# Kernel optimization log

Hardware: AMD Instinct MI355X
Metric: run time of the kernel (lower is better)

## Reference

```python
import jax, jax.numpy as jnp
import numpy as np

T, B, IN, H = 512, 64, 256, 1024
LN_EPS = 1e-5


def _uniform(key, shape, fan_in):
    bound = 1.0 / np.sqrt(fan_in)
    return jax.random.uniform(key, shape, jnp.float32, -bound, bound)


def setup_inputs() -> dict:
    key = jax.random.key(0)
    ks = jax.random.split(key, 8)
    return {
        "x": jax.random.normal(ks[0], (T, B, IN), jnp.float32),
        "Wproj": _uniform(ks[1], (IN, H), IN),          # input_projection (no bias)
        "Wx0": _uniform(ks[2], (IN, 4 * H), IN),        # layer-0 input weights
        "Wh0": _uniform(ks[3], (H, 4 * H), H),          # layer-0 hidden weights
        "b0": _uniform(ks[4], (4 * H,), H),             # combined input+hidden bias
        "Wx1": _uniform(ks[5], (H, 4 * H), H),
        "Wh1": _uniform(ks[6], (H, 4 * H), H),
        "b1": _uniform(ks[7], (4 * H,), H),
        # per-layer LayerNorm params: [num_layers=2, H]
        "lnc_g": jnp.ones((2, H), jnp.float32), "lnc_b": jnp.zeros((2, H), jnp.float32),
        "lnh_g": jnp.ones((2, H), jnp.float32), "lnh_b": jnp.zeros((2, H), jnp.float32),
        "lno_g": jnp.ones((2, H), jnp.float32), "lno_b": jnp.zeros((2, H), jnp.float32),
    }


def _ln(v, g, b):
    m = jnp.mean(v, axis=-1, keepdims=True)
    var = jnp.mean((v - m) ** 2, axis=-1, keepdims=True)
    return (v - m) * jax.lax.rsqrt(var + LN_EPS) * g + b


def reference(x, Wproj, Wx0, Wh0, b0, Wx1, Wh1, b1,
              lnc_g, lnc_b, lnh_g, lnh_b, lno_g, lno_b):
    def cell(inp, h, c, Wx, Wh, bias, l):
        gates = inp @ Wx + h @ Wh + bias            # [B, 4H]
        i, f, g, o = jnp.split(gates, 4, axis=-1)
        c = jax.nn.sigmoid(f) * c + jnp.exp(i) * jnp.tanh(g)  # exponential input gate
        c = _ln(c, lnc_g[l], lnc_b[l])
        h = jax.nn.sigmoid(o) * jnp.tanh(c)
        h = _ln(h, lnh_g[l], lnh_b[l])
        return h, c

    def step(carry, xt):
        h0, c0, h1, c1 = carry
        # layer 0: cell -> residual (projected input) -> outer LayerNorm
        h0, c0 = cell(xt, h0, c0, Wx0, Wh0, b0, 0)
        h0 = _ln(h0 + xt @ Wproj, lno_g[0], lno_b[0])
        # layer 1: cell -> identity residual -> outer LayerNorm
        h1, c1 = cell(h0, h1, c1, Wx1, Wh1, b1, 1)
        h1 = _ln(h1 + h0, lno_g[1], lno_b[1])
        return (h0, c0, h1, c1), h1

    z = jnp.zeros((x.shape[1], H), x.dtype)
    (h0, c0, h1, c1), output = jax.lax.scan(step, (z, z, z, z), x)
    h_final = jnp.stack([h0, h1])  # [num_layers, B, H]
    c_final = jnp.stack([c0, c1])
    return output, h_final, c_final
```

## Files before the change

kernel.cpp:

```cpp
#include <hip/hip_runtime.h>
#include <math.h>

#define TSTEPS 512
#define BSZ    64
#define INDIM  256
#define HDIM   1024
#define G4     4096
#define NX     5120
#define LN_EPS 1e-5f

#define NBLK   256
#define NTHR   1024
#define CHUNK  8
#define CROWS  (CHUNK * BSZ)
#define NCHUNK (TSTEPS / CHUNK)
#define HRING  16
#define HSLOT  65536

#define LDS_LDK    2054
#define LDS_LO_OFF (16 * LDS_LDK)
#define LDS_W_BYTES (2 * 16 * LDS_LDK * 2)
#define LDS_STG_OFF LDS_W_BYTES
#define LDS_RED_OFF (LDS_W_BYTES + 4096)
#define LDS_GST_OFF (LDS_RED_OFF + 256)
#define LDS_BYTES   (LDS_GST_OFF + 16384)

typedef short          s8v __attribute__((ext_vector_type(8)));
typedef float          f4v __attribute__((ext_vector_type(4)));
typedef unsigned short u16;

#define MFMA __builtin_amdgcn_mfma_f32_16x16x32_bf16

__device__ __forceinline__ u16 f2bf(float f) {
    unsigned u = __float_as_uint(f);
    u += 0x7FFFu + ((u >> 16) & 1u);
    return (u16)(u >> 16);
}
__device__ __forceinline__ float bf2f(u16 h) {
    return __uint_as_float(((unsigned)h) << 16);
}
__device__ __forceinline__ float sigm(float x) { return 1.f / (1.f + expf(-x)); }

__device__ __forceinline__ float aldf(const float* p) {
    unsigned v = __hip_atomic_load((unsigned*)p, __ATOMIC_RELAXED,
                                   __HIP_MEMORY_SCOPE_AGENT);
    return __uint_as_float(v);
}
__device__ __forceinline__ void ast16B(u16* p, s8v v) {
    asm volatile("global_store_dwordx4 %0, %1, off sc1"
                 :: "v"(p), "v"(v) : "memory");
}
__device__ __forceinline__ void ast16Bf(float* p, f4v v) {
    asm volatile("global_store_dwordx4 %0, %1, off sc1"
                 :: "v"(p), "v"(v) : "memory");
}

__device__ __forceinline__ void store_c_16B(float* stgw, int lane, f4v acc,
                                            float* dst, int ld)
{
    const int row = lane & 15, kg = lane >> 4;
#pragma unroll
    for (int r = 0; r < 4; ++r)
        stgw[(kg * 4 + r) * 16 + row] = acc[r];
    f4v v = *(f4v*)(stgw + lane * 4);
    ast16Bf(dst + (lane >> 2) * ld + (lane & 3) * 4, v);
}

#define GSTRIDE 512
__device__ __forceinline__ void grid_barrier(int* bar, int nbar, bool fence)
{
    asm volatile("s_waitcnt vmcnt(0)" ::: "memory");
    __syncthreads();
    if (threadIdx.x == 0) {
        const int g = blockIdx.x & 15;
        int* gctr = bar + g * GSTRIDE;
        int* ggo  = gctr + 32;
        int* root = bar + 16 * GSTRIDE;
        int v = __hip_atomic_fetch_add(gctr, 1, __ATOMIC_RELAXED,
                                       __HIP_MEMORY_SCOPE_AGENT);
        if (v == nbar * 16 - 1) {
            int rv = __hip_atomic_fetch_add(root, 1, __ATOMIC_RELAXED,
                                            __HIP_MEMORY_SCOPE_AGENT);
            if (rv == nbar * 16 - 1) {
#pragma unroll
                for (int g2 = 0; g2 < 16; ++g2)
                    __hip_atomic_store(bar + g2 * GSTRIDE + 32, nbar,
                                       __ATOMIC_RELAXED, __HIP_MEMORY_SCOPE_AGENT);
            }
        }
        while (__hip_atomic_load(ggo, __ATOMIC_RELAXED,
                                 __HIP_MEMORY_SCOPE_AGENT) < nbar) {}
        if (fence)
            __builtin_amdgcn_fence(__ATOMIC_ACQUIRE, "agent");
        asm volatile("" ::: "memory");
    }
    __syncthreads();
}

__device__ __forceinline__ void taskA(int g, int lane, float* stgw,
    const u16* __restrict__ h0hi_s, const u16* __restrict__ h0lo_s,
    const u16* __restrict__ Whthi, const u16* __restrict__ Whtlo,
    float* __restrict__ parts0)
{
    const int ks = g & 1, tile = g >> 1;
    const int rt = tile & 3, ct = tile >> 2;
    const int row = lane & 15, kg = lane >> 4;
    const int m = rt * 16 + row;
    const u16* wh = Whthi + (size_t)(ct * 16 + row) * HDIM + ks * 512 + kg * 8;
    const u16* wl = Whtlo + (size_t)(ct * 16 + row) * HDIM + ks * 512 + kg * 8;
    const u16* ah = h0hi_s + (size_t)m * HDIM + ks * 512 + kg * 8;
    const u16* al = h0lo_s + (size_t)m * HDIM + ks * 512 + kg * 8;
    f4v acc = {0.f, 0.f, 0.f, 0.f};
    s8v Ah = *(const s8v*)(ah);
    s8v Al = *(const s8v*)(al);
    s8v Bh = *(const s8v*)(wh);
    s8v Bl = *(const s8v*)(wl);
#pragma unroll
    for (int i = 0; i < 16; ++i) {
        s8v nAh, nAl, nBh, nBl;
        if (i + 1 < 16) {
            const int kn = (i + 1) * 32;
            nAh = *(const s8v*)(ah + kn);
            nAl = *(const s8v*)(al + kn);
            nBh = *(const s8v*)(wh + kn);
            nBl = *(const s8v*)(wl + kn);
        }
        acc = MFMA(Ah, Bh, acc, 0, 0, 0);
        acc = MFMA(Ah, Bl, acc, 0, 0, 0);
        acc = MFMA(Al, Bh, acc, 0, 0, 0);
        Ah = nAh; Al = nAl; Bh = nBh; Bl = nBl;
    }
    store_c_16B(stgw, lane, acc,
                parts0 + (size_t)ks * BSZ * G4 + (size_t)(rt * 16) * G4 + ct * 16,
                G4);
}

__device__ __forceinline__ void taskX(int task, int c, int lane, float* stgw,
    const u16* __restrict__ xhi, const u16* __restrict__ xlo,
    const u16* __restrict__ Wxthi, const u16* __restrict__ Wxtlo,
    float* __restrict__ xgbuf)
{
    const int mt = task & 31, ct = task >> 5;
    const int row = lane & 15, kg = lane >> 4;
    const int mr = mt * 16 + row;
    const u16* ah = xhi + ((size_t)c * CROWS + mr) * INDIM + kg * 8;
    const u16* al = xlo + ((size_t)c * CROWS + mr) * INDIM + kg * 8;
    const u16* wh = Wxthi + (size_t)(ct * 16 + row) * INDIM + kg * 8;
    const u16* wl = Wxtlo + (size_t)(ct * 16 + row) * INDIM + kg * 8;
    f4v acc = {0.f, 0.f, 0.f, 0.f};
    s8v Ah = *(const s8v*)(ah);
    s8v Al = *(const s8v*)(al);
    s8v Bh = *(const s8v*)(wh);
    s8v Bl = *(const s8v*)(wl);
#pragma unroll
    for (int i = 0; i < 8; ++i) {
        s8v nAh, nAl, nBh, nBl;
        if (i + 1 < 8) {
            const int kn = (i + 1) * 32;
            nAh = *(const s8v*)(ah + kn);
            nAl = *(const s8v*)(al + kn);
            nBh = *(const s8v*)(wh + kn);
            nBl = *(const s8v*)(wl + kn);
        }
        acc = MFMA(Ah, Bh, acc, 0, 0, 0);
        acc = MFMA(Ah, Bl, acc, 0, 0, 0);
        acc = MFMA(Al, Bh, acc, 0, 0, 0);
        Ah = nAh; Al = nAl; Bh = nBh; Bl = nBl;
    }
    store_c_16B(stgw, lane, acc,
                xgbuf + (size_t)(mt * 16) * NX + ct * 16, NX);
}

__device__ __forceinline__ void taskC(int blk, int wv, int lane, float* stgw,
    const u16* __restrict__ shW,
    const u16* __restrict__ h0hi_s, const u16* __restrict__ h0lo_s,
    const u16* __restrict__ h1hi_s, const u16* __restrict__ h1lo_s,
    float* __restrict__ parts1)
{
    const int rt = wv & 3, hs = wv >> 2;
    const int row = lane & 15, kg = lane >> 4;
    const int m = rt * 16 + row;
    const u16* ah0 = (hs ? h1hi_s : h0hi_s) + (size_t)m * HDIM + kg * 8;
    const u16* al0 = (hs ? h1lo_s : h0lo_s) + (size_t)m * HDIM + kg * 8;
    const u16* sh  = shW + row * LDS_LDK + hs * 1024 + kg * 8;
    const u16* sl  = shW + LDS_LO_OFF + row * LDS_LDK + hs * 1024 + kg * 8;
    f4v acc = {0.f, 0.f, 0.f, 0.f};
    s8v Ah = *(const s8v*)(ah0);
    s8v Al = *(const s8v*)(al0);
#pragma unroll
    for (int i = 0; i < 32; ++i) {
        s8v nAh, nAl;
        if (i + 1 < 32) {
            nAh = *(const s8v*)(ah0 + (i + 1) * 32);
            nAl = *(const s8v*)(al0 + (i + 1) * 32);
        }
        const int kloc = i * 32;
        s8v Bh = *(const s8v*)(sh + kloc);
        s8v Bl = *(const s8v*)(sl + kloc);
        acc = MFMA(Ah, Bh, acc, 0, 0, 0);
        acc = MFMA(Ah, Bl, acc, 0, 0, 0);
        acc = MFMA(Al, Bh, acc, 0, 0, 0);
        Ah = nAh; Al = nAl;
    }
    store_c_16B(stgw, lane, acc,
                parts1 + (size_t)hs * BSZ * G4 + (size_t)(rt * 16) * G4 + blk * 16,
                G4);
}

__device__ __forceinline__ float2 blk_sum2(float s, float q, float* red, int tid)
{
#pragma unroll
    for (int off = 32; off; off >>= 1) {
        s += __shfl_down(s, off);
        q += __shfl_down(q, off);
    }
    if ((tid & 63) == 0) { red[(tid >> 6) * 2] = s; red[(tid >> 6) * 2 + 1] = q; }
    __syncthreads();
    float ts = 0.f, tq = 0.f;
#pragma unroll
    for (int i = 0; i < 16; ++i) { ts += red[2 * i]; tq += red[2 * i + 1]; }
    __syncthreads();
    return make_float2(ts, tq);
}

__device__ __forceinline__ float lnorm(float v, float2 sq, float g, float b)
{
    float mean = sq.x * (1.f / 1024.f);
    float var  = sq.y * (1.f / 1024.f) - mean * mean;
    return (v - mean) * rsqrtf(var + LN_EPS) * g + b;
}

__device__ __forceinline__ void store_h_16B(u16* stg, int tid,
                                            u16 hi, u16 lo,
                                            u16* dhi, u16* dlo, int base)
{
    stg[tid] = hi;
    stg[1024 + tid] = lo;
    __syncthreads();
    if (tid < 256) {
        const u16* src = stg + (tid >> 7) * 1024 + (tid & 127) * 8;
        s8v v = *(const s8v*)src;
        u16* dst = ((tid >> 7) == 0 ? dhi : dlo) + base + (tid & 127) * 8;
        ast16B(dst, v);
    }
    __syncthreads();
}

__global__ __launch_bounds__(NTHR, 4) void persistent(
    const u16* __restrict__ xhi,  const u16* __restrict__ xlo,
    const u16* __restrict__ Whthi, const u16* __restrict__ Whtlo,
    const u16* __restrict__ Wxthi, const u16* __restrict__ Wxtlo,
    const u16* __restrict__ W1thi, const u16* __restrict__ W1tlo,
    const float* __restrict__ b0, const float* __restrict__ b1,
    const float* __restrict__ lncg, const float* __restrict__ lncb,
    const float* __restrict__ lnhg, const float* __restrict__ lnhb,
    const float* __restrict__ lnog, const float* __restrict__ lnob,
    float* __restrict__ xg,
    float* __restrict__ parts0,
    float* __restrict__ parts1,
    u16* __restrict__ h0hi, u16* __restrict__ h0lo,
    u16* __restrict__ h1hi, u16* __restrict__ h1lo,
    float* __restrict__ out, int* bar)
{
    extern __shared__ char smem[];
    u16*   shW   = (u16*)smem;
    u16*   stg   = (u16*)(smem + LDS_STG_OFF);
    float* red   = (float*)(smem + LDS_RED_OFF);
    float* stg_g = (float*)(smem + LDS_GST_OFF);

    const int blk  = blockIdx.x;
    const int tid  = threadIdx.x;
    const int wv   = tid >> 6;
    const int lane = tid & 63;
    float* stgw = stg_g + wv * 256;
    int nbar = 0;

    float c0reg = 0.f, h0reg = 0.f, c1reg = 0.f, h1reg = 0.f;

    {
        const size_t gcol = (size_t)(blk * 16 + wv) * 2048;
        for (int j = lane * 8; j < 2048; j += 512) {
            *(s8v*)(shW + wv * LDS_LDK + j)              = *(const s8v*)(W1thi + gcol + j);
            *(s8v*)(shW + LDS_LO_OFF + wv * LDS_LDK + j) = *(const s8v*)(W1tlo + gcol + j);
        }
    }
    grid_barrier(bar, ++nbar, false);

    {
        const int g = blk * 16 + wv;
        for (int task = g; task < 10240; task += 4096)
            taskX(task, 0, lane, stgw, xhi, xlo, Wxthi, Wxtlo, xg);
    }
    grid_barrier(bar, ++nbar, false);

    for (int t = 0; t < TSTEPS; ++t) {
        const int s0  = t & (HRING - 1);
        const int s0p = (t - 1) & (HRING - 1);
        const int s1p = (t - 1) & (HRING - 1);
        const bool fence = ((t & 7) == 7);

        if (blk < 64) {
            const int b = blk, n = tid;
            const float* XG = xg + (size_t)((t >> 3) & 1) * CROWS * NX
                                 + (size_t)((t & 7) * BSZ + b) * NX;
            const float* P0 = parts0 + (size_t)b * G4;
            const float* P1 = parts0 + (size_t)(BSZ + b) * G4;
            float gi = aldf(&XG[n])        + aldf(&P0[n])        + aldf(&P1[n])        + b0[n];
            float gf = aldf(&XG[1024 + n]) + aldf(&P0[1024 + n]) + aldf(&P1[1024 + n]) + b0[1024 + n];
            float gg = aldf(&XG[2048 + n]) + aldf(&P0[2048 + n]) + aldf(&P1[2048 + n]) + b0[2048 + n];
            float go = aldf(&XG[3072 + n]) + aldf(&P0[3072 + n]) + aldf(&P1[3072 + n]) + b0[3072 + n];
            float xp = aldf(&XG[4096 + n]);
            float cv = sigm(gf) * c0reg + expf(gi) * tanhf(gg);
            float2 r = blk_sum2(cv, cv * cv, red, tid);
            float cl = lnorm(cv, r, lncg[n], lncb[n]);
            c0reg = cl;
            float hv = sigm(go) * tanhf(cl);
            r = blk_sum2(hv, hv * hv, red, tid);
            float hl = lnorm(hv, r, lnhg[n], lnhb[n]) + xp;
            r = blk_sum2(hl, hl * hl, red, tid);
            float hn = lnorm(hl, r, lnog[n], lnob[n]);
            h0reg = hn;
            u16 hi = f2bf(hn);
            store_h_16B(stg, tid, hi, f2bf(hn - bf2f(hi)),
                        h0hi + (size_t)s0 * HSLOT, h0lo + (size_t)s0 * HSLOT,
                        b * HDIM);
        } else if (blk < 128) {
            if (t > 0) {
                const int b = blk - 64, n = tid;
                const float* P0 = parts1 + (size_t)b * G4;
                const float* P1 = parts1 + (size_t)(BSZ + b) * G4;
                float gi = aldf(&P0[n])        + aldf(&P1[n])        + b1[n];
                float gf = aldf(&P0[1024 + n]) + aldf(&P1[1024 + n]) + b1[1024 + n];
                float gg = aldf(&P0[2048 + n]) + aldf(&P1[2048 + n]) + b1[2048 + n];
                float go = aldf(&P0[3072 + n]) + aldf(&P1[3072 + n]) + b1[3072 + n];
                float cv = sigm(gf) * c1reg + expf(gi) * tanhf(gg);
                float2 r = blk_sum2(cv, cv * cv, red, tid);
                float cl = lnorm(cv, r, lncg[HDIM + n], lncb[HDIM + n]);
                c1reg = cl;
                float hv = sigm(go) * tanhf(cl);
                r = blk_sum2(hv, hv * hv, red, tid);
                float h0v = bf2f(h0hi[(size_t)s0p * HSLOT + b * HDIM + n])
                          + bf2f(h0lo[(size_t)s0p * HSLOT + b * HDIM + n]);
                float hl = lnorm(hv, r, lnhg[HDIM + n], lnhb[HDIM + n]) + h0v;
                r = blk_sum2(hl, hl * hl, red, tid);
                float hn = lnorm(hl, r, lnog[HDIM + n], lnob[HDIM + n]);
                h1reg = hn;
                u16 hi = f2bf(hn);
                out[(size_t)(t - 1) * BSZ * HDIM + b * HDIM + n] = hn;
                store_h_16B(stg, tid, hi, f2bf(hn - bf2f(hi)),
                            h1hi + (size_t)s1p * HSLOT, h1lo + (size_t)s1p * HSLOT,
                            b * HDIM);
            }
        } else {
            const int c = (t >> 3) + 1;
            if (c < NCHUNK) {
                float* xgbuf = xg + (size_t)(c & 1) * CROWS * NX;
                const int widx = (blk - 128) * 16 + wv;
                if (widx < 1280)
                    taskX((t & 7) * 1280 + widx, c, lane, stgw,
                          xhi, xlo, Wxthi, Wxtlo, xgbuf);
            }
        }
        grid_barrier(bar, ++nbar, false);

        if (wv < 8) {
            taskC(blk, wv, lane, stgw, shW,
                  h0hi + (size_t)s0 * HSLOT,  h0lo + (size_t)s0 * HSLOT,
                  h1hi + (size_t)s1p * HSLOT, h1lo + (size_t)s1p * HSLOT,
                  parts1);
        } else if (t + 1 < TSTEPS) {
            taskA(blk * 8 + (wv - 8), lane, stgw,
                  h0hi + (size_t)s0 * HSLOT, h0lo + (size_t)s0 * HSLOT,
                  Whthi, Whtlo, parts0);
        }
        grid_barrier(bar, ++nbar, fence);
    }

    if (blk >= 64 && blk < 128) {
        const int b = blk - 64, n = tid;
        const int tp = TSTEPS - 1;
        const int sp = tp & (HRING - 1);
        const float* P0 = parts1 + (size_t)b * G4;
        const float* P1 = parts1 + (size_t)(BSZ + b) * G4;
        float gi = aldf(&P0[n])        + aldf(&P1[n])        + b1[n];
        float gf = aldf(&P0[1024 + n]) + aldf(&P1[1024 + n]) + b1[1024 + n];
        float gg = aldf(&P0[2048 + n]) + aldf(&P1[2048 + n]) + b1[2048 + n];
        float go = aldf(&P0[3072 + n]) + aldf(&P1[3072 + n]) + b1[3072 + n];
        float cv = sigm(gf) * c1reg + expf(gi) * tanhf(gg);
        float2 r = blk_sum2(cv, cv * cv, red, tid);
        float cl = lnorm(cv, r, lncg[HDIM + n], lncb[HDIM + n]);
        c1reg = cl;
        float hv = sigm(go) * tanhf(cl);
        r = blk_sum2(hv, hv * hv, red, tid);
        float h0v = bf2f(h0hi[(size_t)sp * HSLOT + b * HDIM + n])
                  + bf2f(h0lo[(size_t)sp * HSLOT + b * HDIM + n]);
        float hl = lnorm(hv, r, lnhg[HDIM + n], lnhb[HDIM + n]) + h0v;
        r = blk_sum2(hl, hl * hl, red, tid);
        float hn = lnorm(hl, r, lnog[HDIM + n], lnob[HDIM + n]);
        h1reg = hn;
        out[(size_t)tp * BSZ * HDIM + b * HDIM + n] = hn;
    }

    {
        const size_t F = (size_t)TSTEPS * BSZ * HDIM;
        if (blk < 64) {
            out[F +          blk * HDIM + tid] = h0reg;
            out[F + 131072 + blk * HDIM + tid] = c0reg;
        } else if (blk < 128) {
            const int b = blk - 64;
            out[F +  65536 + b * HDIM + tid] = h1reg;
            out[F + 196608 + b * HDIM + tid] = c1reg;
        }
    }
}

__global__ __launch_bounds__(256) void transpose_split(
    const float* __restrict__ src, int N,
    u16* __restrict__ dsthi, u16* __restrict__ dstlo,
    int ldd, int noff, int koff)
{
    __shared__ float tile[32][33];
    const int n0 = blockIdx.x * 32, k0 = blockIdx.y * 32;
    const int tx = threadIdx.x & 31, ty = threadIdx.x >> 5;
#pragma unroll
    for (int i = 0; i < 4; ++i)
        tile[ty + i * 8][tx] = src[(size_t)(k0 + ty + i * 8) * N + n0 + tx];
    __syncthreads();
#pragma unroll
    for (int i = 0; i < 4; ++i) {
        float v = tile[tx][ty + i * 8];
        u16 hi = f2bf(v);
        u16 lo = f2bf(v - bf2f(hi));
        size_t idx = (size_t)(n0 + ty + i * 8 + noff) * ldd + k0 + koff + tx;
        dsthi[idx] = hi;
        dstlo[idx] = lo;
    }
}

__global__ void conv_split(const float* __restrict__ src,
                           u16* __restrict__ hi, u16* __restrict__ lo, int n4)
{
    int i = blockIdx.x * 256 + threadIdx.x;
    if (i < n4) {
        float4 v = ((const float4*)src)[i];
        ushort4 h, l;
        h.x = f2bf(v.x); l.x = f2bf(v.x - bf2f(h.x));
        h.y = f2bf(v.y); l.y = f2bf(v.y - bf2f(h.y));
        h.z = f2bf(v.z); l.z = f2bf(v.z - bf2f(h.z));
        h.w = f2bf(v.w); l.w = f2bf(v.w - bf2f(h.w));
        ((ushort4*)hi)[i] = h;
        ((ushort4*)lo)[i] = l;
    }
}

extern "C" void kernel_launch(void* const* d_in, const int* in_sizes, int n_in,
                              void* d_out, int out_size, void* d_ws, size_t ws_size,
                              hipStream_t stream)
{
    const float* x     = (const float*)d_in[0];
    const float* Wproj = (const float*)d_in[1];
    const float* Wx0   = (const float*)d_in[2];
    const float* Wh0   = (const float*)d_in[3];
    const float* b0    = (const float*)d_in[4];
    const float* Wx1   = (const float*)d_in[5];
    const float* Wh1   = (const float*)d_in[6];
    const float* b1    = (const float*)d_in[7];
    const float* lnc_g = (const float*)d_in[8];
    const float* lnc_b = (const float*)d_in[9];
    const float* lnh_g = (const float*)d_in[10];
    const float* lnh_b = (const float*)d_in[11];
    const float* lno_g = (const float*)d_in[12];
    const float* lno_b = (const float*)d_in[13];
    float* out = (float*)d_out;

    char* base = (char*)d_ws;
    size_t o = 0;
    u16* x_hi  = (u16*)(base + o); o += (size_t)TSTEPS * BSZ * INDIM * 2;
    u16* x_lo  = (u16*)(base + o); o += (size_t)TSTEPS * BSZ * INDIM * 2;
    u16* Whthi = (u16*)(base + o); o += (size_t)G4 * HDIM * 2;
    u16* Whtlo = (u16*)(base + o); o += (size_t)G4 * HDIM * 2;
    u16* Wxthi = (u16*)(base + o); o += (size_t)NX * INDIM * 2;
    u16* Wxtlo = (u16*)(base + o); o += (size_t)NX * INDIM * 2;
    u16* W1thi = (u16*)(base + o); o += (size_t)G4 * 2048 * 2;
    u16* W1tlo = (u16*)(base + o); o += (size_t)G4 * 2048 * 2;
    float* xg     = (float*)(base + o); o += (size_t)2 * CROWS * NX * 4;
    float* parts0 = (float*)(base + o); o += (size_t)2 * BSZ * G4 * 4;
    float* parts1 = (float*)(base + o); o += (size_t)2 * BSZ * G4 * 4;
    u16* h0hi = (u16*)(base + o); o += (size_t)HRING * HSLOT * 2;
    u16* h0lo = (u16*)(base + o); o += (size_t)HRING * HSLOT * 2;
    u16* h1hi = (u16*)(base + o); o += (size_t)HRING * HSLOT * 2;
    u16* h1lo = (u16*)(base + o); o += (size_t)HRING * HSLOT * 2;
    int* bar  = (int*)(base + o); o += 40960;
    if (ws_size < o) return;

    conv_split<<<dim3(8192), 256, 0, stream>>>(x, x_hi, x_lo, 2097152);
    transpose_split<<<dim3(128, 32), 256, 0, stream>>>(Wh0, G4, Whthi, Whtlo, HDIM, 0, 0);
    transpose_split<<<dim3(128, 8),  256, 0, stream>>>(Wx0,   G4,   Wxthi, Wxtlo, INDIM, 0,    0);
    transpose_split<<<dim3(32, 8),   256, 0, stream>>>(Wproj, HDIM, Wxthi, Wxtlo, INDIM, 4096, 0);
    transpose_split<<<dim3(128, 32), 256, 0, stream>>>(Wx1, G4, W1thi, W1tlo, 2048, 0, 0);
    transpose_split<<<dim3(128, 32), 256, 0, stream>>>(Wh1, G4, W1thi, W1tlo, 2048, 0, 1024);
    hipMemsetAsync(parts0, 0, (size_t)2 * BSZ * G4 * 4, stream);
    hipMemsetAsync(h0hi, 0, (size_t)4 * HRING * HSLOT * 2, stream);
    hipMemsetAsync(bar, 0, 40960, stream);

    persistent<<<dim3(NBLK), dim3(NTHR), LDS_BYTES, stream>>>(
        x_hi, x_lo, Whthi, Whtlo, Wxthi, Wxtlo, W1thi, W1tlo, b0, b1,
        lnc_g, lnc_b, lnh_g, lnh_b, lno_g, lno_b,
        xg, parts0, parts1,
        h0hi, h0lo, h1hi, h1lo, out, bar);
}
```

Measured before the change: 25.35 ms.

## Drop split-K partials and fold x-projection tasks into the MFMA phase

The recurrent matmuls for both layers now have each wave compute the full K dimension into a single partial buffer, instead of two split-K halves. The elementwise phase therefore loads one partial per gate rather than two. The x-gate precompute work moves from the blocks that were idle during elementwise (blocks 128+) onto waves 8-15 of every block in the matmul phase. This frees those waves' time and removes the extra partial reads. The cost is longer per-wave MFMA chains and less parallelism per tile. Memory fences now run every 16 steps instead of every 8, and the output write uses nontemporal stores.

```diff
diff --git a/kernel.cpp b/kernel.cpp
--- a/kernel.cpp
+++ b/kernel.cpp
@@ -97,28 +97,26 @@
     __syncthreads();
 }
 
-__device__ __forceinline__ void taskA(int g, int lane, float* stgw,
+__device__ __forceinline__ void taskA(int blk, int rt, int lane, float* stgw,
     const u16* __restrict__ h0hi_s, const u16* __restrict__ h0lo_s,
     const u16* __restrict__ Whthi, const u16* __restrict__ Whtlo,
     float* __restrict__ parts0)
 {
-    const int ks = g & 1, tile = g >> 1;
-    const int rt = tile & 3, ct = tile >> 2;
     const int row = lane & 15, kg = lane >> 4;
     const int m = rt * 16 + row;
-    const u16* wh = Whthi + (size_t)(ct * 16 + row) * HDIM + ks * 512 + kg * 8;
-    const u16* wl = Whtlo + (size_t)(ct * 16 + row) * HDIM + ks * 512 + kg * 8;
-    const u16* ah = h0hi_s + (size_t)m * HDIM + ks * 512 + kg * 8;
-    const u16* al = h0lo_s + (size_t)m * HDIM + ks * 512 + kg * 8;
+    const u16* wh = Whthi + (size_t)(blk * 16 + row) * HDIM + kg * 8;
+    const u16* wl = Whtlo + (size_t)(blk * 16 + row) * HDIM + kg * 8;
+    const u16* ah = h0hi_s + (size_t)m * HDIM + kg * 8;
+    const u16* al = h0lo_s + (size_t)m * HDIM + kg * 8;
     f4v acc = {0.f, 0.f, 0.f, 0.f};
     s8v Ah = *(const s8v*)(ah);
     s8v Al = *(const s8v*)(al);
     s8v Bh = *(const s8v*)(wh);
     s8v Bl = *(const s8v*)(wl);
 #pragma unroll
-    for (int i = 0; i < 16; ++i) {
+    for (int i = 0; i < 32; ++i) {
         s8v nAh, nAl, nBh, nBl;
-        if (i + 1 < 16) {
+        if (i + 1 < 32) {
             const int kn = (i + 1) * 32;
             nAh = *(const s8v*)(ah + kn);
             nAl = *(const s8v*)(al + kn);
@@ -131,8 +129,7 @@
         Ah = nAh; Al = nAl; Bh = nBh; Bl = nBl;
     }
     store_c_16B(stgw, lane, acc,
-                parts0 + (size_t)ks * BSZ * G4 + (size_t)(rt * 16) * G4 + ct * 16,
-                G4);
+                parts0 + (size_t)(rt * 16) * G4 + blk * 16, G4);
 }
 
 __device__ __forceinline__ void taskX(int task, int c, int lane, float* stgw,
@@ -171,40 +168,41 @@
                 xgbuf + (size_t)(mt * 16) * NX + ct * 16, NX);
 }
 
-__device__ __forceinline__ void taskC(int blk, int wv, int lane, float* stgw,
+__device__ __forceinline__ void taskC(int blk, int rt, int lane, float* stgw,
     const u16* __restrict__ shW,
     const u16* __restrict__ h0hi_s, const u16* __restrict__ h0lo_s,
     const u16* __restrict__ h1hi_s, const u16* __restrict__ h1lo_s,
     float* __restrict__ parts1)
 {
-    const int rt = wv & 3, hs = wv >> 2;
     const int row = lane & 15, kg = lane >> 4;
     const int m = rt * 16 + row;
-    const u16* ah0 = (hs ? h1hi_s : h0hi_s) + (size_t)m * HDIM + kg * 8;
-    const u16* al0 = (hs ? h1lo_s : h0lo_s) + (size_t)m * HDIM + kg * 8;
-    const u16* sh  = shW + row * LDS_LDK + hs * 1024 + kg * 8;
-    const u16* sl  = shW + LDS_LO_OFF + row * LDS_LDK + hs * 1024 + kg * 8;
     f4v acc = {0.f, 0.f, 0.f, 0.f};
-    s8v Ah = *(const s8v*)(ah0);
-    s8v Al = *(const s8v*)(al0);
-#pragma unroll
-    for (int i = 0; i < 32; ++i) {
-        s8v nAh, nAl;
-        if (i + 1 < 32) {
-            nAh = *(const s8v*)(ah0 + (i + 1) * 32);
-            nAl = *(const s8v*)(al0 + (i + 1) * 32);
-        }
-        const int kloc = i * 32;
-        s8v Bh = *(const s8v*)(sh + kloc);
-        s8v Bl = *(const s8v*)(sl + kloc);
-        acc = MFMA(Ah, Bh, acc, 0, 0, 0);
-        acc = MFMA(Ah, Bl, acc, 0, 0, 0);
-        acc = MFMA(Al, Bh, acc, 0, 0, 0);
-        Ah = nAh; Al = nAl;
+#pragma unroll
+    for (int hs = 0; hs < 2; ++hs) {
+        const u16* ah0 = (hs ? h1hi_s : h0hi_s) + (size_t)m * HDIM + kg * 8;
+        const u16* al0 = (hs ? h1lo_s : h0lo_s) + (size_t)m * HDIM + kg * 8;
+        const u16* sh  = shW + row * LDS_LDK + hs * 1024 + kg * 8;
+        const u16* sl  = shW + LDS_LO_OFF + row * LDS_LDK + hs * 1024 + kg * 8;
+        s8v Ah = *(const s8v*)(ah0);
+        s8v Al = *(const s8v*)(al0);
+#pragma unroll
+        for (int i = 0; i < 32; ++i) {
+            s8v nAh, nAl;
+            if (i + 1 < 32) {
+                nAh = *(const s8v*)(ah0 + (i + 1) * 32);
+                nAl = *(const s8v*)(al0 + (i + 1) * 32);
+            }
+            const int kloc = i * 32;
+            s8v Bh = *(const s8v*)(sh + kloc);
+            s8v Bl = *(const s8v*)(sl + kloc);
+            acc = MFMA(Ah, Bh, acc, 0, 0, 0);
+            acc = MFMA(Ah, Bl, acc, 0, 0, 0);
+            acc = MFMA(Al, Bh, acc, 0, 0, 0);
+            Ah = nAh; Al = nAl;
+        }
     }
     store_c_16B(stgw, lane, acc,
-                parts1 + (size_t)hs * BSZ * G4 + (size_t)(rt * 16) * G4 + blk * 16,
-                G4);
+                parts1 + (size_t)(rt * 16) * G4 + blk * 16, G4);
 }
 
 __device__ __forceinline__ float2 blk_sum2(float s, float q, float* red, int tid)
@@ -296,19 +294,17 @@
     for (int t = 0; t < TSTEPS; ++t) {
         const int s0  = t & (HRING - 1);
         const int s0p = (t - 1) & (HRING - 1);
-        const int s1p = (t - 1) & (HRING - 1);
-        const bool fence = ((t & 7) == 7);
+        const bool fence = ((t & 15) == 15);
 
         if (blk < 64) {
             const int b = blk, n = tid;
             const float* XG = xg + (size_t)((t >> 3) & 1) * CROWS * NX
                                  + (size_t)((t & 7) * BSZ + b) * NX;
             const float* P0 = parts0 + (size_t)b * G4;
-            const float* P1 = parts0 + (size_t)(BSZ + b) * G4;
-            float gi = aldf(&XG[n])        + aldf(&P0[n])        + aldf(&P1[n])        + b0[n];
-            float gf = aldf(&XG[1024 + n]) + aldf(&P0[1024 + n]) + aldf(&P1[1024 + n]) + b0[1024 + n];
-            float gg = aldf(&XG[2048 + n]) + aldf(&P0[2048 + n]) + aldf(&P1[2048 + n]) + b0[2048 + n];
-            float go = aldf(&XG[3072 + n]) + aldf(&P0[3072 + n]) + aldf(&P1[3072 + n]) + b0[3072 + n];
+            float gi = aldf(&XG[n])        + aldf(&P0[n])        + b0[n];
+            float gf = aldf(&XG[1024 + n]) + aldf(&P0[1024 + n]) + b0[1024 + n];
+            float gg = aldf(&XG[2048 + n]) + aldf(&P0[2048 + n]) + b0[2048 + n];
+            float go = aldf(&XG[3072 + n]) + aldf(&P0[3072 + n]) + b0[3072 + n];
             float xp = aldf(&XG[4096 + n]);
             float cv = sigm(gf) * c0reg + expf(gi) * tanhf(gg);
             float2 r = blk_sum2(cv, cv * cv, red, tid);
@@ -324,54 +320,52 @@
             store_h_16B(stg, tid, hi, f2bf(hn - bf2f(hi)),
                         h0hi + (size_t)s0 * HSLOT, h0lo + (size_t)s0 * HSLOT,
                         b * HDIM);
-        } else if (blk < 128) {
-            if (t > 0) {
-                const int b = blk - 64, n = tid;
-                const float* P0 = parts1 + (size_t)b * G4;
-                const float* P1 = parts1 + (size_t)(BSZ + b) * G4;
-                float gi = aldf(&P0[n])        + aldf(&P1[n])        + b1[n];
-                float gf = aldf(&P0[1024 + n]) + aldf(&P1[1024 + n]) + b1[1024 + n];
-                float gg = aldf(&P0[2048 + n]) + aldf(&P1[2048 + n]) + b1[2048 + n];
-                float go = aldf(&P0[3072 + n]) + aldf(&P1[3072 + n]) + b1[3072 + n];
-                float cv = sigm(gf) * c1reg + expf(gi) * tanhf(gg);
-                float2 r = blk_sum2(cv, cv * cv, red, tid);
-                float cl = lnorm(cv, r, lncg[HDIM + n], lncb[HDIM + n]);
-                c1reg = cl;
-                float hv = sigm(go) * tanhf(cl);
-                r = blk_sum2(hv, hv * hv, red, tid);
-                float h0v = bf2f(h0hi[(size_t)s0p * HSLOT + b * HDIM + n])
-                          + bf2f(h0lo[(size_t)s0p * HSLOT + b * HDIM + n]);
-                float hl = lnorm(hv, r, lnhg[HDIM + n], lnhb[HDIM + n]) + h0v;
-                r = blk_sum2(hl, hl * hl, red, tid);
-                float hn = lnorm(hl, r, lnog[HDIM + n], lnob[HDIM + n]);
-                h1reg = hn;
-                u16 hi = f2bf(hn);
-                out[(size_t)(t - 1) * BSZ * HDIM + b * HDIM + n] = hn;
-                store_h_16B(stg, tid, hi, f2bf(hn - bf2f(hi)),
-                            h1hi + (size_t)s1p * HSLOT, h1lo + (size_t)s1p * HSLOT,
-                            b * HDIM);
-            }
+        } else if (blk < 128 && t > 0) {
+            const int b = blk - 64, n = tid;
+            const float* P0 = parts1 + (size_t)b * G4;
+            float gi = aldf(&P0[n])        + b1[n];
+            float gf = aldf(&P0[1024 + n]) + b1[1024 + n];
+            float gg = aldf(&P0[2048 + n]) + b1[2048 + n];
+            float go = aldf(&P0[3072 + n]) + b1[3072 + n];
+            float cv = sigm(gf) * c1reg + expf(gi) * tanhf(gg);
+            float2 r = blk_sum2(cv, cv * cv, red, tid);
+            float cl = lnorm(cv, r, lncg[HDIM + n], lncb[HDIM + n]);
+            c1reg = cl;
+            float hv = sigm(go) * tanhf(cl);
+            r = blk_sum2(hv, hv * hv, red, tid);
+            float h0v = bf2f(h0hi[(size_t)s0p * HSLOT + b * HDIM + n])
+                      + bf2f(h0lo[(size_t)s0p * HSLOT + b * HDIM + n]);
+            float hl = lnorm(hv, r, lnhg[HDIM + n], lnhb[HDIM + n]) + h0v;
+            r = blk_sum2(hl, hl * hl, red, tid);
+            float hn = lnorm(hl, r, lnog[HDIM + n], lnob[HDIM + n]);
+            h1reg = hn;
+            u16 hi = f2bf(hn);
+            __builtin_nontemporal_store(hn, &out[(size_t)(t - 1) * BSZ * HDIM + b * HDIM + n]);
+            store_h_16B(stg, tid, hi, f2bf(hn - bf2f(hi)),
+                        h1hi + (size_t)s0p * HSLOT, h1lo + (size_t)s0p * HSLOT,
+                        b * HDIM);
+        }
+        grid_barrier(bar, ++nbar, false);
+
+        if (wv < 4) {
+            taskC(blk, wv, lane, stgw, shW,
+                  h0hi + (size_t)s0 * HSLOT,  h0lo + (size_t)s0 * HSLOT,
+                  h1hi + (size_t)s0p * HSLOT, h1lo + (size_t)s0p * HSLOT,
+                  parts1);
+        } else if (wv < 8) {
+            if (t + 1 < TSTEPS)
+                taskA(blk, wv - 4, lane, stgw,
+                      h0hi + (size_t)s0 * HSLOT, h0lo + (size_t)s0 * HSLOT,
+                      Whthi, Whtlo, parts0);
         } else {
             const int c = (t >> 3) + 1;
             if (c < NCHUNK) {
                 float* xgbuf = xg + (size_t)(c & 1) * CROWS * NX;
-                const int widx = (blk - 128) * 16 + wv;
+                const int widx = blk * 8 + (wv - 8);
                 if (widx < 1280)
                     taskX((t & 7) * 1280 + widx, c, lane, stgw,
                           xhi, xlo, Wxthi, Wxtlo, xgbuf);
             }
-        }
-        grid_barrier(bar, ++nbar, false);
-
-        if (wv < 8) {
-            taskC(blk, wv, lane, stgw, shW,
-                  h0hi + (size_t)s0 * HSLOT,  h0lo + (size_t)s0 * HSLOT,
-                  h1hi + (size_t)s1p * HSLOT, h1lo + (size_t)s1p * HSLOT,
-                  parts1);
-        } else if (t + 1 < TSTEPS) {
-            taskA(blk * 8 + (wv - 8), lane, stgw,
-                  h0hi + (size_t)s0 * HSLOT, h0lo + (size_t)s0 * HSLOT,
-                  Whthi, Whtlo, parts0);
         }
         grid_barrier(bar, ++nbar, fence);
     }
@@ -381,11 +375,10 @@
         const int tp = TSTEPS - 1;
         const int sp = tp & (HRING - 1);
         const float* P0 = parts1 + (size_t)b * G4;
-        const float* P1 = parts1 + (size_t)(BSZ + b) * G4;
-        float gi = aldf(&P0[n])        + aldf(&P1[n])        + b1[n];
-        float gf = aldf(&P0[1024 + n]) + aldf(&P1[1024 + n]) + b1[1024 + n];
-        float gg = aldf(&P0[2048 + n]) + aldf(&P1[2048 + n]) + b1[2048 + n];
-        float go = aldf(&P0[3072 + n]) + aldf(&P1[3072 + n]) + b1[3072 + n];
+        float gi = aldf(&P0[n])        + b1[n];
+        float gf = aldf(&P0[1024 + n]) + b1[1024 + n];
+        float gg = aldf(&P0[2048 + n]) + b1[2048 + n];
+        float go = aldf(&P0[3072 + n]) + b1[3072 + n];
         float cv = sigm(gf) * c1reg + expf(gi) * tanhf(gg);
         float2 r = blk_sum2(cv, cv * cv, red, tid);
         float cl = lnorm(cv, r, lncg[HDIM + n], lncb[HDIM + n]);
@@ -484,8 +477,8 @@
     u16* W1thi = (u16*)(base + o); o += (size_t)G4 * 2048 * 2;
     u16* W1tlo = (u16*)(base + o); o += (size_t)G4 * 2048 * 2;
     float* xg     = (float*)(base + o); o += (size_t)2 * CROWS * NX * 4;
-    float* parts0 = (float*)(base + o); o += (size_t)2 * BSZ * G4 * 4;
-    float* parts1 = (float*)(base + o); o += (size_t)2 * BSZ * G4 * 4;
+    float* parts0 = (float*)(base + o); o += (size_t)BSZ * G4 * 4;
+    float* parts1 = (float*)(base + o); o += (size_t)BSZ * G4 * 4;
     u16* h0hi = (u16*)(base + o); o += (size_t)HRING * HSLOT * 2;
     u16* h0lo = (u16*)(base + o); o += (size_t)HRING * HSLOT * 2;
     u16* h1hi = (u16*)(base + o); o += (size_t)HRING * HSLOT * 2;
@@ -499,7 +492,7 @@
     transpose_split<<<dim3(32, 8),   256, 0, stream>>>(Wproj, HDIM, Wxthi, Wxtlo, INDIM, 4096, 0);
     transpose_split<<<dim3(128, 32), 256, 0, stream>>>(Wx1, G4, W1thi, W1tlo, 2048, 0, 0);
     transpose_split<<<dim3(128, 32), 256, 0, stream>>>(Wh1, G4, W1thi, W1tlo, 2048, 0, 1024);
-    hipMemsetAsync(parts0, 0, (size_t)2 * BSZ * G4 * 4, stream);
+    hipMemsetAsync(parts0, 0, (size_t)BSZ * G4 * 4, stream);
     hipMemsetAsync(h0hi, 0, (size_t)4 * HRING * HSLOT * 2, stream);
     hipMemsetAsync(bar, 0, 40960, stream);
 
```

Result: faster. 24.33 ms, median of 2 (-4.0%).

## Repartition persistent LSTM work: dedicated layer-1 matmul blocks, skewed two-phase schedule

Applied to the files above, without the earlier changes.

Restructures the persistent grid's per-step schedule. Blocks 64-191 now own the layer-1 gate matmul, with only the hi half of W1 cached in LDS (32 columns per block) and the lo half streamed from global memory. The layer-0 recurrent matmul (taskA) moves to 2048 waves spread over the other blocks in the second phase, and the input-projection work goes to the remaining blocks. Layer 1 is skewed by one step inside a single loop of TSTEPS+1 iterations, which removes the separate epilogue, and the agent fence runs less often. The intent is to balance phase loads across blocks and shorten the critical path per barrier. In exchange, layer-1 lo weights are re-read from global memory every step and the fence interval doubles.

```diff
diff --git a/kernel.cpp b/kernel.cpp
--- a/kernel.cpp
+++ b/kernel.cpp
@@ -18,7 +18,6 @@
 #define HSLOT  65536
 
 #define LDS_LDK    2054
-#define LDS_LO_OFF (16 * LDS_LDK)
 #define LDS_W_BYTES (2 * 16 * LDS_LDK * 2)
 #define LDS_STG_OFF LDS_W_BYTES
 #define LDS_RED_OFF (LDS_W_BYTES + 4096)
@@ -97,13 +96,12 @@
     __syncthreads();
 }
 
-__device__ __forceinline__ void taskA(int g, int lane, float* stgw,
+__device__ __forceinline__ void taskA(int t, int lane, float* stgw,
     const u16* __restrict__ h0hi_s, const u16* __restrict__ h0lo_s,
     const u16* __restrict__ Whthi, const u16* __restrict__ Whtlo,
     float* __restrict__ parts0)
 {
-    const int ks = g & 1, tile = g >> 1;
-    const int rt = tile & 3, ct = tile >> 2;
+    const int ks = t & 1, rt = (t >> 1) & 3, ct = t >> 3;
     const int row = lane & 15, kg = lane >> 4;
     const int m = rt * 16 + row;
     const u16* wh = Whthi + (size_t)(ct * 16 + row) * HDIM + ks * 512 + kg * 8;
@@ -172,38 +170,40 @@
 }
 
 __device__ __forceinline__ void taskC(int blk, int wv, int lane, float* stgw,
-    const u16* __restrict__ shW,
+    const u16* __restrict__ shW, const u16* __restrict__ W1tlo,
     const u16* __restrict__ h0hi_s, const u16* __restrict__ h0lo_s,
     const u16* __restrict__ h1hi_s, const u16* __restrict__ h1lo_s,
     float* __restrict__ parts1)
 {
-    const int rt = wv & 3, hs = wv >> 2;
+    const int s = wv >> 3, hs = (wv >> 2) & 1, rt = wv & 3;
+    const int ct = 2 * (blk - 64) + s;
     const int row = lane & 15, kg = lane >> 4;
     const int m = rt * 16 + row;
     const u16* ah0 = (hs ? h1hi_s : h0hi_s) + (size_t)m * HDIM + kg * 8;
     const u16* al0 = (hs ? h1lo_s : h0lo_s) + (size_t)m * HDIM + kg * 8;
-    const u16* sh  = shW + row * LDS_LDK + hs * 1024 + kg * 8;
-    const u16* sl  = shW + LDS_LO_OFF + row * LDS_LDK + hs * 1024 + kg * 8;
+    const u16* sh  = shW + (size_t)(s * 16 + row) * LDS_LDK + hs * 1024 + kg * 8;
+    const u16* wl  = W1tlo + (size_t)(ct * 16 + row) * 2048 + hs * 1024 + kg * 8;
     f4v acc = {0.f, 0.f, 0.f, 0.f};
     s8v Ah = *(const s8v*)(ah0);
     s8v Al = *(const s8v*)(al0);
+    s8v Bl = *(const s8v*)(wl);
 #pragma unroll
     for (int i = 0; i < 32; ++i) {
-        s8v nAh, nAl;
+        s8v nAh, nAl, nBl;
         if (i + 1 < 32) {
-            nAh = *(const s8v*)(ah0 + (i + 1) * 32);
-            nAl = *(const s8v*)(al0 + (i + 1) * 32);
-        }
-        const int kloc = i * 32;
-        s8v Bh = *(const s8v*)(sh + kloc);
-        s8v Bl = *(const s8v*)(sl + kloc);
+            const int kn = (i + 1) * 32;
+            nAh = *(const s8v*)(ah0 + kn);
+            nAl = *(const s8v*)(al0 + kn);
+            nBl = *(const s8v*)(wl + kn);
+        }
+        s8v Bh = *(const s8v*)(sh + i * 32);
         acc = MFMA(Ah, Bh, acc, 0, 0, 0);
         acc = MFMA(Ah, Bl, acc, 0, 0, 0);
         acc = MFMA(Al, Bh, acc, 0, 0, 0);
-        Ah = nAh; Al = nAl;
+        Ah = nAh; Al = nAl; Bl = nBl;
     }
     store_c_16B(stgw, lane, acc,
-                parts1 + (size_t)hs * BSZ * G4 + (size_t)(rt * 16) * G4 + blk * 16,
+                parts1 + (size_t)hs * BSZ * G4 + (size_t)(rt * 16) * G4 + ct * 16,
                 G4);
 }
 
@@ -277,11 +277,14 @@
 
     float c0reg = 0.f, h0reg = 0.f, c1reg = 0.f, h1reg = 0.f;
 
-    {
-        const size_t gcol = (size_t)(blk * 16 + wv) * 2048;
-        for (int j = lane * 8; j < 2048; j += 512) {
-            *(s8v*)(shW + wv * LDS_LDK + j)              = *(const s8v*)(W1thi + gcol + j);
-            *(s8v*)(shW + LDS_LO_OFF + wv * LDS_LDK + j) = *(const s8v*)(W1tlo + gcol + j);
+    if (blk >= 64 && blk < 192) {
+        const int s = wv >> 3;
+        const int ct = 2 * (blk - 64) + s;
+        for (int cc = wv & 7; cc < 16; cc += 8) {
+            const size_t gcol = (size_t)(ct * 16 + cc) * 2048;
+            for (int j = lane * 8; j < 2048; j += 512)
+                *(s8v*)(shW + (size_t)(s * 16 + cc) * LDS_LDK + j) =
+                    *(const s8v*)(W1thi + gcol + j);
         }
     }
     grid_barrier(bar, ++nbar, false);
@@ -293,39 +296,61 @@
     }
     grid_barrier(bar, ++nbar, false);
 
-    for (int t = 0; t < TSTEPS; ++t) {
-        const int s0  = t & (HRING - 1);
-        const int s0p = (t - 1) & (HRING - 1);
-        const int s1p = (t - 1) & (HRING - 1);
-        const bool fence = ((t & 7) == 7);
+    for (int u = 0; u <= TSTEPS; ++u) {
+        const int s0  = u & (HRING - 1);
+        const int sA0 = (u - 1) & (HRING - 1);
+        const int sA1 = (u - 2) & (HRING - 1);
+        const bool fence = ((u & 15) == 15);
 
         if (blk < 64) {
-            const int b = blk, n = tid;
-            const float* XG = xg + (size_t)((t >> 3) & 1) * CROWS * NX
-                                 + (size_t)((t & 7) * BSZ + b) * NX;
-            const float* P0 = parts0 + (size_t)b * G4;
-            const float* P1 = parts0 + (size_t)(BSZ + b) * G4;
-            float gi = aldf(&XG[n])        + aldf(&P0[n])        + aldf(&P1[n])        + b0[n];
-            float gf = aldf(&XG[1024 + n]) + aldf(&P0[1024 + n]) + aldf(&P1[1024 + n]) + b0[1024 + n];
-            float gg = aldf(&XG[2048 + n]) + aldf(&P0[2048 + n]) + aldf(&P1[2048 + n]) + b0[2048 + n];
-            float go = aldf(&XG[3072 + n]) + aldf(&P0[3072 + n]) + aldf(&P1[3072 + n]) + b0[3072 + n];
-            float xp = aldf(&XG[4096 + n]);
-            float cv = sigm(gf) * c0reg + expf(gi) * tanhf(gg);
-            float2 r = blk_sum2(cv, cv * cv, red, tid);
-            float cl = lnorm(cv, r, lncg[n], lncb[n]);
-            c0reg = cl;
-            float hv = sigm(go) * tanhf(cl);
-            r = blk_sum2(hv, hv * hv, red, tid);
-            float hl = lnorm(hv, r, lnhg[n], lnhb[n]) + xp;
-            r = blk_sum2(hl, hl * hl, red, tid);
-            float hn = lnorm(hl, r, lnog[n], lnob[n]);
-            h0reg = hn;
-            u16 hi = f2bf(hn);
-            store_h_16B(stg, tid, hi, f2bf(hn - bf2f(hi)),
-                        h0hi + (size_t)s0 * HSLOT, h0lo + (size_t)s0 * HSLOT,
-                        b * HDIM);
-        } else if (blk < 128) {
-            if (t > 0) {
+            if (u < TSTEPS) {
+                const int b = blk, n = tid;
+                const float* XG = xg + (size_t)((u >> 3) & 1) * CROWS * NX
+                                     + (size_t)((u & 7) * BSZ + b) * NX;
+                const float* P0 = parts0 + (size_t)b * G4;
+                const float* P1 = parts0 + (size_t)(BSZ + b) * G4;
+                float gi = aldf(&XG[n])        + aldf(&P0[n])        + aldf(&P1[n])        + b0[n];
+                float gf = aldf(&XG[1024 + n]) + aldf(&P0[1024 + n]) + aldf(&P1[1024 + n]) + b0[1024 + n];
+                float gg = aldf(&XG[2048 + n]) + aldf(&P0[2048 + n]) + aldf(&P1[2048 + n]) + b0[2048 + n];
+                float go = aldf(&XG[3072 + n]) + aldf(&P0[3072 + n]) + aldf(&P1[3072 + n]) + b0[3072 + n];
+                float xp = aldf(&XG[4096 + n]);
+                float cv = sigm(gf) * c0reg + expf(gi) * tanhf(gg);
+                float2 r = blk_sum2(cv, cv * cv, red, tid);
+                float cl = lnorm(cv, r, lncg[n], lncb[n]);
+                c0reg = cl;
+                float hv = sigm(go) * tanhf(cl);
+                r = blk_sum2(hv, hv * hv, red, tid);
+                float hl = lnorm(hv, r, lnhg[n], lnhb[n]) + xp;
+                r = blk_sum2(hl, hl * hl, red, tid);
+                float hn = lnorm(hl, r, lnog[n], lnob[n]);
+                h0reg = hn;
+                u16 hi = f2bf(hn);
+                store_h_16B(stg, tid, hi, f2bf(hn - bf2f(hi)),
+                            h0hi + (size_t)s0 * HSLOT, h0lo + (size_t)s0 * HSLOT,
+                            blk * HDIM);
+            }
+        } else if (blk < 192) {
+            if (u >= 1)
+                taskC(blk, wv, lane, stgw, shW, W1tlo,
+                      h0hi + (size_t)sA0 * HSLOT, h0lo + (size_t)sA0 * HSLOT,
+                      h1hi + (size_t)sA1 * HSLOT, h1lo + (size_t)sA1 * HSLOT,
+                      parts1);
+        } else {
+            const int c = (u >> 3) + 1;
+            if (c < NCHUNK && u < TSTEPS) {
+                float* xgbuf = xg + (size_t)(c & 1) * CROWS * NX;
+                const int widx = (blk - 192) * 16 + wv;
+                taskX((u & 7) * 1280 + widx, c, lane, stgw,
+                      xhi, xlo, Wxthi, Wxtlo, xgbuf);
+                if (widx + 1024 < 1280)
+                    taskX((u & 7) * 1280 + widx + 1024, c, lane, stgw,
+                          xhi, xlo, Wxthi, Wxtlo, xgbuf);
+            }
+        }
+        grid_barrier(bar, ++nbar, false);
+
+        if (blk >= 64 && blk < 128) {
+            if (u >= 1) {
                 const int b = blk - 64, n = tid;
                 const float* P0 = parts1 + (size_t)b * G4;
                 const float* P1 = parts1 + (size_t)(BSZ + b) * G4;
@@ -339,66 +364,28 @@
                 c1reg = cl;
                 float hv = sigm(go) * tanhf(cl);
                 r = blk_sum2(hv, hv * hv, red, tid);
-                float h0v = bf2f(h0hi[(size_t)s0p * HSLOT + b * HDIM + n])
-                          + bf2f(h0lo[(size_t)s0p * HSLOT + b * HDIM + n]);
+                float h0v = bf2f(h0hi[(size_t)sA0 * HSLOT + b * HDIM + n])
+                          + bf2f(h0lo[(size_t)sA0 * HSLOT + b * HDIM + n]);
                 float hl = lnorm(hv, r, lnhg[HDIM + n], lnhb[HDIM + n]) + h0v;
                 r = blk_sum2(hl, hl * hl, red, tid);
                 float hn = lnorm(hl, r, lnog[HDIM + n], lnob[HDIM + n]);
                 h1reg = hn;
                 u16 hi = f2bf(hn);
-                out[(size_t)(t - 1) * BSZ * HDIM + b * HDIM + n] = hn;
+                __builtin_nontemporal_store(hn,
+                    &out[(size_t)(u - 1) * BSZ * HDIM + b * HDIM + n]);
                 store_h_16B(stg, tid, hi, f2bf(hn - bf2f(hi)),
-                            h1hi + (size_t)s1p * HSLOT, h1lo + (size_t)s1p * HSLOT,
+                            h1hi + (size_t)sA0 * HSLOT, h1lo + (size_t)sA0 * HSLOT,
                             b * HDIM);
             }
-        } else {
-            const int c = (t >> 3) + 1;
-            if (c < NCHUNK) {
-                float* xgbuf = xg + (size_t)(c & 1) * CROWS * NX;
-                const int widx = (blk - 128) * 16 + wv;
-                if (widx < 1280)
-                    taskX((t & 7) * 1280 + widx, c, lane, stgw,
-                          xhi, xlo, Wxthi, Wxtlo, xgbuf);
-            }
-        }
-        grid_barrier(bar, ++nbar, false);
-
-        if (wv < 8) {
-            taskC(blk, wv, lane, stgw, shW,
-                  h0hi + (size_t)s0 * HSLOT,  h0lo + (size_t)s0 * HSLOT,
-                  h1hi + (size_t)s1p * HSLOT, h1lo + (size_t)s1p * HSLOT,
-                  parts1);
-        } else if (t + 1 < TSTEPS) {
-            taskA(blk * 8 + (wv - 8), lane, stgw,
-                  h0hi + (size_t)s0 * HSLOT, h0lo + (size_t)s0 * HSLOT,
-                  Whthi, Whtlo, parts0);
+        } else if (u + 1 < TSTEPS) {
+            const int idx = (blk < 64) ? blk : (blk - 64);
+            const int t = idx * 16 + wv;
+            if (t < 2048)
+                taskA(t, lane, stgw,
+                      h0hi + (size_t)s0 * HSLOT, h0lo + (size_t)s0 * HSLOT,
+                      Whthi, Whtlo, parts0);
         }
         grid_barrier(bar, ++nbar, fence);
-    }
-
-    if (blk >= 64 && blk < 128) {
-        const int b = blk - 64, n = tid;
-        const int tp = TSTEPS - 1;
-        const int sp = tp & (HRING - 1);
-        const float* P0 = parts1 + (size_t)b * G4;
-        const float* P1 = parts1 + (size_t)(BSZ + b) * G4;
-        float gi = aldf(&P0[n])        + aldf(&P1[n])        + b1[n];
-        float gf = aldf(&P0[1024 + n]) + aldf(&P1[1024 + n]) + b1[1024 + n];
-        float gg = aldf(&P0[2048 + n]) + aldf(&P1[2048 + n]) + b1[2048 + n];
-        float go = aldf(&P0[3072 + n]) + aldf(&P1[3072 + n]) + b1[3072 + n];
-        float cv = sigm(gf) * c1reg + expf(gi) * tanhf(gg);
-        float2 r = blk_sum2(cv, cv * cv, red, tid);
-        float cl = lnorm(cv, r, lncg[HDIM + n], lncb[HDIM + n]);
-        c1reg = cl;
-        float hv = sigm(go) * tanhf(cl);
-        r = blk_sum2(hv, hv * hv, red, tid);
-        float h0v = bf2f(h0hi[(size_t)sp * HSLOT + b * HDIM + n])
-                  + bf2f(h0lo[(size_t)sp * HSLOT + b * HDIM + n]);
-        float hl = lnorm(hv, r, lnhg[HDIM + n], lnhb[HDIM + n]) + h0v;
-        r = blk_sum2(hl, hl * hl, red, tid);
-        float hn = lnorm(hl, r, lnog[HDIM + n], lnob[HDIM + n]);
-        h1reg = hn;
-        out[(size_t)tp * BSZ * HDIM + b * HDIM + n] = hn;
     }
 
     {
```

New measurement: 38.41 ms. 51.5% more time.
